# Performance work log

Measured on AMD Instinct MI355X. Metric: run time of the kernel, lower is better.

## Reference

```python
import jax, jax.numpy as jnp
import numpy as np

N_HEAD = 16
N_QUERY_GROUPS = 4
HEAD_SIZE = 128
ROPE_N_ELEM = 32
N_EMBD = 2048
LN_EPS = 1e-5


def _layernorm(x, w, b):
    mu = jnp.mean(x, axis=-1, keepdims=True)
    var = jnp.var(x, axis=-1, keepdims=True)
    return (x - mu) * jax.lax.rsqrt(var + LN_EPS) * w + b


def _apply_rope(x, cos, sin):
    # x: (B, H, T, ROPE_N_ELEM); cos/sin: (T, ROPE_N_ELEM) broadcast over B,H
    half = x.shape[-1] // 2
    x1, x2 = x[..., :half], x[..., half:]
    rotated = jnp.concatenate((-x2, x1), axis=-1)
    return x * cos + rotated * sin


def setup_inputs() -> dict:
    key = jax.random.key(0)
    ks = jax.random.split(key, 12)
    B, T, C = 2, 2048, N_EMBD
    qkv_out = (N_HEAD + 2 * N_QUERY_GROUPS) * HEAD_SIZE
    ffn = 4 * C
    s = lambda fan_in: 1.0 / np.sqrt(fan_in)
    # rope cache (lit-gpt build_rope_cache, base 10000)
    theta = 1.0 / (10000.0 ** (jnp.arange(0, ROPE_N_ELEM, 2, dtype=jnp.float32) / ROPE_N_ELEM))
    idx_theta = jnp.outer(jnp.arange(T, dtype=jnp.float32), theta)  # (T, ROPE/2)
    idx_theta = jnp.concatenate((idx_theta, idx_theta), axis=-1)    # (T, ROPE)
    return {
        'x': jax.random.normal(ks[0], (B, T, C), dtype=jnp.float32),
        'cos': jnp.cos(idx_theta),
        'sin': jnp.sin(idx_theta),
        'ln1_w': jnp.ones((C,), jnp.float32),
        'ln1_b': jnp.zeros((C,), jnp.float32),
        'w_qkv': jax.random.normal(ks[1], (C, qkv_out), jnp.float32) * s(C),
        'b_qkv': jnp.zeros((qkv_out,), jnp.float32),
        'w_proj': jax.random.normal(ks[2], (C, C), jnp.float32) * s(C),
        'b_proj': jnp.zeros((C,), jnp.float32),
        'ln2_w': jnp.ones((C,), jnp.float32),
        'ln2_b': jnp.zeros((C,), jnp.float32),
        'w_fc1': jax.random.normal(ks[3], (C, ffn), jnp.float32) * s(C),
        'b_fc1': jnp.zeros((ffn,), jnp.float32),
        'w_fc2': jax.random.normal(ks[4], (ffn, C), jnp.float32) * s(ffn),
        'b_fc2': jnp.zeros((C,), jnp.float32),
    }


def reference(x, cos, sin, ln1_w, ln1_b, w_qkv, b_qkv, w_proj, b_proj,
              ln2_w, ln2_b, w_fc1, b_fc1, w_fc2, b_fc2):
    B, T, C = x.shape
    q_per_kv = N_HEAD // N_QUERY_GROUPS
    D = HEAD_SIZE

    # LayerNormLinear: fused LN + QKV projection
    qkv = _layernorm(x, ln1_w, ln1_b) @ w_qkv + b_qkv           # (B,T,(H+2G)*D)
    qkv = qkv.reshape(B, T, N_QUERY_GROUPS, q_per_kv + 2, D)
    qkv = jnp.transpose(qkv, (0, 2, 3, 1, 4))                    # (B,G,q_per_kv+2,T,D)
    q = qkv[:, :, :q_per_kv]                                     # (B,G,q_per_kv,T,D)
    k = qkv[:, :, q_per_kv:q_per_kv + 1]                         # (B,G,1,T,D)
    v = qkv[:, :, q_per_kv + 1:]
    k = jnp.broadcast_to(k, (B, N_QUERY_GROUPS, q_per_kv, T, D))
    v = jnp.broadcast_to(v, (B, N_QUERY_GROUPS, q_per_kv, T, D))
    q = q.reshape(B, N_HEAD, T, D)
    k = k.reshape(B, N_HEAD, T, D)
    v = v.reshape(B, N_HEAD, T, D)

    # inline RoPE on first ROPE_N_ELEM channels
    q = jnp.concatenate((_apply_rope(q[..., :ROPE_N_ELEM], cos, sin), q[..., ROPE_N_ELEM:]), axis=-1)
    k = jnp.concatenate((_apply_rope(k[..., :ROPE_N_ELEM], cos, sin), k[..., ROPE_N_ELEM:]), axis=-1)

    # causal scaled dot-product attention
    scale = 1.0 / jnp.sqrt(jnp.asarray(D, q.dtype))
    scores = jnp.einsum('bhtd,bhsd->bhts', q, k) * scale          # (B,H,T,T)
    causal = jnp.tril(jnp.ones((T, T), dtype=bool))
    scores = jnp.where(causal, scores, jnp.finfo(scores.dtype).min)
    probs = jax.nn.softmax(scores, axis=-1)
    y = jnp.einsum('bhts,bhsd->bhtd', probs, v)                   # (B,H,T,D)
    y = jnp.transpose(y, (0, 2, 1, 3)).reshape(B, T, C)

    h = y @ w_proj + b_proj

    # parallel residual: x + attn + LayerNormMLP(x)
    mlp_in = _layernorm(x, ln2_w, ln2_b)
    mlp = jax.nn.gelu(mlp_in @ w_fc1 + b_fc1, approximate=False) @ w_fc2 + b_fc2
    return mlp + h + x
```

## Files before the change

### kernel.cpp

```cpp
#include <hip/hip_runtime.h>
#include <cstdint>
#include <cstddef>


typedef unsigned short u16;
typedef __bf16 bf16x8 __attribute__((ext_vector_type(8)));
typedef float  f32x4  __attribute__((ext_vector_type(4)));

#define B_      2
#define T_      2048
#define C_      2048
#define NH_     16
#define NG_     4
#define HD_     128
#define QKVO_   3072
#define FFN_    8192
#define ROWS_   4096

__device__ __forceinline__ u16 f2b(float f) {
  union { float f; uint32_t u; } c; c.f = f;
  uint32_t u = c.u;
  return (u16)((u + 0x7fffu + ((u >> 16) & 1u)) >> 16);
}
__device__ __forceinline__ float b2f(u16 h) {
  union { uint32_t u; float f; } c; c.u = ((uint32_t)h) << 16;
  return c.f;
}
__device__ __forceinline__ void load_lds16(const void* g, void* l) {
  __builtin_amdgcn_global_load_lds(
      (const __attribute__((address_space(1))) uint32_t*)g,
      (__attribute__((address_space(3))) uint32_t*)l, 16, 0, 0);
}

__global__ __launch_bounds__(256) void ln2x_kernel(
    const float* __restrict__ x,
    const float* __restrict__ w1, const float* __restrict__ b1,
    const float* __restrict__ w2, const float* __restrict__ b2,
    u16* __restrict__ o1, u16* __restrict__ o2)
{
  const int row = blockIdx.x;
  const float4* xr = (const float4*)(x + (size_t)row * C_);
  const int t = threadIdx.x;
  float4 v0 = xr[t];
  float4 v1 = xr[t + 256];
  float s  = v0.x + v0.y + v0.z + v0.w + v1.x + v1.y + v1.z + v1.w;
  float ss = v0.x*v0.x + v0.y*v0.y + v0.z*v0.z + v0.w*v0.w
           + v1.x*v1.x + v1.y*v1.y + v1.z*v1.z + v1.w*v1.w;
#pragma unroll
  for (int o = 32; o; o >>= 1) { s += __shfl_down(s, o); ss += __shfl_down(ss, o); }
  __shared__ float red[8];
  const int w = t >> 6;
  if ((t & 63) == 0) { red[w] = s; red[4 + w] = ss; }
  __syncthreads();
  s  = red[0] + red[1] + red[2] + red[3];
  ss = red[4] + red[5] + red[6] + red[7];
  const float mu   = s * (1.0f / C_);
  const float rstd = rsqrtf(ss * (1.0f / C_) - mu * mu + 1e-5f);

  const float4* W1 = (const float4*)w1; const float4* B1 = (const float4*)b1;
  const float4* W2 = (const float4*)w2; const float4* B2 = (const float4*)b2;
#pragma unroll
  for (int c = 0; c < 2; ++c) {
    const int idx = t + c * 256;
    float4 v = (c == 0) ? v0 : v1;
    float n0 = (v.x - mu) * rstd, n1 = (v.y - mu) * rstd;
    float n2 = (v.z - mu) * rstd, n3 = (v.w - mu) * rstd;
    float4 a1 = W1[idx], c1 = B1[idx], a2 = W2[idx], c2 = B2[idx];
    uint64_t p1 = (uint64_t)f2b(n0*a1.x + c1.x)
                | ((uint64_t)f2b(n1*a1.y + c1.y) << 16)
                | ((uint64_t)f2b(n2*a1.z + c1.z) << 32)
                | ((uint64_t)f2b(n3*a1.w + c1.w) << 48);
    uint64_t p2 = (uint64_t)f2b(n0*a2.x + c2.x)
                | ((uint64_t)f2b(n1*a2.y + c2.y) << 16)
                | ((uint64_t)f2b(n2*a2.z + c2.z) << 32)
                | ((uint64_t)f2b(n3*a2.w + c2.w) << 48);
    ((uint64_t*)o1)[(size_t)row * (C_/4) + idx] = p1;
    ((uint64_t*)o2)[(size_t)row * (C_/4) + idx] = p2;
  }
}

__global__ __launch_bounds__(256) void tcast64(
    const float* __restrict__ in, u16* __restrict__ out, int R, int Ccols)
{
  __shared__ u16 tileT[64 * 72];
  const int c0 = blockIdx.x * 64, r0 = blockIdx.y * 64;
  const int lin = threadIdx.x;
  {
    const int cI = (lin & 15) * 4, r = lin >> 4;
#pragma unroll
    for (int i = 0; i < 4; ++i) {
      const int rr = r + i * 16;
      float4 v = *(const float4*)(in + (size_t)(r0 + rr) * Ccols + c0 + cI);
      tileT[(cI + 0) * 72 + rr] = f2b(v.x);
      tileT[(cI + 1) * 72 + rr] = f2b(v.y);
      tileT[(cI + 2) * 72 + rr] = f2b(v.z);
      tileT[(cI + 3) * 72 + rr] = f2b(v.w);
    }
  }
  __syncthreads();
  {
    const int rr = (lin & 15) * 4, cc = lin >> 4;
#pragma unroll
    for (int i = 0; i < 4; ++i) {
      const int c = cc + i * 16;
      ushort4 pk = *(const ushort4*)(tileT + c * 72 + rr);
      *(ushort4*)(out + (size_t)(c0 + c) * R + r0 + rr) = pk;
    }
  }
}

__device__ __forceinline__ void gemm_loop(
    const u16* __restrict__ Ap, const u16* __restrict__ Bp,
    int K, int kbeg, int kend, f32x4 acc[4][4])
{
  __shared__ u16 As[128 * 32];
  __shared__ u16 Bs[128 * 32];
  const int tid = threadIdx.x;
  const int w = tid >> 6, lane = tid & 63, quad = lane >> 4, l16 = lane & 15;
  const int wm = w >> 1, wn = w & 1;
  const int rowS = tid >> 2, slotS = tid & 3;

  for (int k0 = kbeg; k0 < kend; k0 += 32) {
    __syncthreads();
#pragma unroll
    for (int i = 0; i < 2; ++i) {
      int row = rowS + i * 64;
      int chunk = slotS ^ ((row >> 1) & 3);
      load_lds16(Ap + (size_t)row * K + k0 + chunk * 8, (char*)As + i * 4096 + w * 1024);
      load_lds16(Bp + (size_t)row * K + k0 + chunk * 8, (char*)Bs + i * 4096 + w * 1024);
    }
    __syncthreads();

    bf16x8 af[4], bf[4];
#pragma unroll
    for (int mt = 0; mt < 4; ++mt) {
      int row = wm * 64 + mt * 16 + l16;
      int slot = quad ^ ((row >> 1) & 3);
      af[mt] = *(const bf16x8*)(As + row * 32 + slot * 8);
    }
#pragma unroll
    for (int nt = 0; nt < 4; ++nt) {
      int row = wn * 64 + nt * 16 + l16;
      int slot = quad ^ ((row >> 1) & 3);
      bf[nt] = *(const bf16x8*)(Bs + row * 32 + slot * 8);
    }
#pragma unroll
    for (int mt = 0; mt < 4; ++mt)
#pragma unroll
      for (int nt = 0; nt < 4; ++nt)
        acc[mt][nt] = __builtin_amdgcn_mfma_f32_16x16x32_bf16(af[mt], bf[nt], acc[mt][nt], 0, 0, 0);
  }
}

#define GEMM_PROLOGUE(KSTRIDE, KBEG, KEND)                                    \
  const int tid = threadIdx.x;                                                \
  const int w = tid >> 6, lane = tid & 63, quad = lane >> 4, l16 = lane & 15; \
  const int wm = w >> 1, wn = w & 1;                                          \
  const int m0 = blockIdx.y * 128, n0 = blockIdx.x * 128;                     \
  const f32x4 vzero = {0.f, 0.f, 0.f, 0.f};                                   \
  f32x4 acc[4][4];                                                            \
  _Pragma("unroll") for (int i = 0; i < 4; ++i)                               \
    _Pragma("unroll") for (int j = 0; j < 4; ++j) acc[i][j] = vzero;          \
  gemm_loop(A + (size_t)m0 * (KSTRIDE), Bt + (size_t)n0 * (KSTRIDE),          \
            (KSTRIDE), (KBEG), (KEND), acc);

__global__ __launch_bounds__(256, 2) void gemm_qkv(
    const u16* __restrict__ A, const u16* __restrict__ Bt,
    const float* __restrict__ bias,
    const float* __restrict__ cosb, const float* __restrict__ sinb,
    u16* __restrict__ qb, u16* __restrict__ kb, u16* __restrict__ vtb)
{
  GEMM_PROLOGUE(C_, 0, C_)
  const int slice = n0 >> 7;
  const int g = slice / 6, s = slice % 6;
  const int b = m0 >> 11;

#pragma unroll
  for (int mt = 0; mt < 4; ++mt) {
    const int rowbase = m0 + wm * 64 + mt * 16 + quad * 4;
    const int t0 = rowbase & 2047;
    float vv[4][4];
#pragma unroll
    for (int nt = 0; nt < 4; ++nt)
#pragma unroll
      for (int r = 0; r < 4; ++r)
        vv[nt][r] = acc[mt][nt][r] + bias[n0 + wn * 64 + nt * 16 + l16];

    if (s < 5 && wn == 0) {
#pragma unroll
      for (int r = 0; r < 4; ++r) {
        const int t = t0 + r;
        float cs0 = cosb[t * 32 + l16],      sn0 = sinb[t * 32 + l16];
        float cs1 = cosb[t * 32 + 16 + l16], sn1 = sinb[t * 32 + 16 + l16];
        float a = vv[0][r], c = vv[1][r];
        vv[0][r] = a * cs0 - c * sn0;
        vv[1][r] = c * cs1 + a * sn1;
      }
    }

    if (s < 4) {
      u16* dst = qb + (size_t)(b * NH_ + g * 4 + s) * T_ * HD_;
#pragma unroll
      for (int nt = 0; nt < 4; ++nt)
#pragma unroll
        for (int r = 0; r < 4; ++r)
          dst[(size_t)(t0 + r) * HD_ + wn * 64 + nt * 16 + l16] = f2b(vv[nt][r]);
    } else if (s == 4) {
      u16* dst = kb + (size_t)(b * NG_ + g) * T_ * HD_;
#pragma unroll
      for (int nt = 0; nt < 4; ++nt)
#pragma unroll
        for (int r = 0; r < 4; ++r)
          dst[(size_t)(t0 + r) * HD_ + wn * 64 + nt * 16 + l16] = f2b(vv[nt][r]);
    } else {
      u16* dst = vtb + (size_t)(b * NG_ + g) * HD_ * T_;
#pragma unroll
      for (int nt = 0; nt < 4; ++nt) {
        const int d = wn * 64 + nt * 16 + l16;
        ushort4 pk = { f2b(vv[nt][0]), f2b(vv[nt][1]), f2b(vv[nt][2]), f2b(vv[nt][3]) };
        *(ushort4*)(dst + (size_t)d * T_ + t0) = pk;
      }
    }
  }
}

__global__ __launch_bounds__(256, 2) void gemm_proj(
    const u16* __restrict__ A, const u16* __restrict__ Bt,
    const float* __restrict__ bias, const float* __restrict__ resid,
    float* __restrict__ outF)
{
  GEMM_PROLOGUE(C_, 0, C_)
#pragma unroll
  for (int mt = 0; mt < 4; ++mt)
#pragma unroll
    for (int nt = 0; nt < 4; ++nt)
#pragma unroll
      for (int r = 0; r < 4; ++r) {
        int row = m0 + wm * 64 + mt * 16 + quad * 4 + r;
        int col = n0 + wn * 64 + nt * 16 + l16;
        float v = acc[mt][nt][r] + bias[col] + resid[(size_t)row * C_ + col];
        outF[(size_t)row * C_ + col] = v;
      }
}

__global__ __launch_bounds__(256, 2) void gemm_fc1(
    const u16* __restrict__ A, const u16* __restrict__ Bt,
    const float* __restrict__ bias, u16* __restrict__ outB)
{
  GEMM_PROLOGUE(C_, 0, C_)
#pragma unroll
  for (int mt = 0; mt < 4; ++mt)
#pragma unroll
    for (int nt = 0; nt < 4; ++nt)
#pragma unroll
      for (int r = 0; r < 4; ++r) {
        int row = m0 + wm * 64 + mt * 16 + quad * 4 + r;
        int col = n0 + wn * 64 + nt * 16 + l16;
        float v = acc[mt][nt][r] + bias[col];
        v = 0.5f * v * (1.0f + erff(v * 0.70710678118654752f));
        outB[(size_t)row * FFN_ + col] = f2b(v);
      }
}

__global__ __launch_bounds__(256, 2) void gemm_fc2(
    const u16* __restrict__ A, const u16* __restrict__ Bt,
    const float* __restrict__ bias, float* __restrict__ outF,
    float* __restrict__ pbuf)
{
  const int kh = FFN_ / 2;
  const int kbeg = blockIdx.z * kh;
  GEMM_PROLOGUE(FFN_, kbeg, kbeg + kh)
#pragma unroll
  for (int mt = 0; mt < 4; ++mt)
#pragma unroll
    for (int nt = 0; nt < 4; ++nt)
#pragma unroll
      for (int r = 0; r < 4; ++r) {
        int row = m0 + wm * 64 + mt * 16 + quad * 4 + r;
        int col = n0 + wn * 64 + nt * 16 + l16;
        size_t idx = (size_t)row * C_ + col;
        if (blockIdx.z == 0)
          outF[idx] = acc[mt][nt][r] + bias[col] + outF[idx];
        else
          pbuf[idx] = acc[mt][nt][r];
      }
}

__global__ __launch_bounds__(256) void add_pbuf(
    float* __restrict__ out, const float* __restrict__ p)
{
  size_t i = ((size_t)blockIdx.x * 256 + threadIdx.x) * 4;
  float4 a = *(float4*)(out + i);
  float4 b = *(const float4*)(p + i);
  a.x += b.x; a.y += b.y; a.z += b.z; a.w += b.w;
  *(float4*)(out + i) = a;
}

__global__ __launch_bounds__(256, 2) void attn_kernel(
    const u16* __restrict__ qb, const u16* __restrict__ kb,
    const u16* __restrict__ vt, u16* __restrict__ y)
{
  __shared__ u16 Qs[64 * 128];
  __shared__ u16 Ks[64 * 128];
  __shared__ u16 Vs[128 * 64];
  __shared__ u16 Ps[4 * 16 * 64];

  const int tid = threadIdx.x;
  const int w = tid >> 6, lane = tid & 63, quad = lane >> 4, l16 = lane & 15;
  const int b = blockIdx.y >> 4, h = blockIdx.y & 15, g = h >> 2;
  const int q0 = blockIdx.x * 64;

  const u16* Qg = qb + (size_t)(b * NH_ + h) * T_ * HD_;
  const u16* Kg = kb + (size_t)(b * NG_ + g) * T_ * HD_;
  const u16* Vg = vt + (size_t)(b * NG_ + g) * HD_ * T_;

  {
    const int row = tid >> 4, slot = tid & 15;
#pragma unroll
    for (int i = 0; i < 4; ++i) {
      int r = row + i * 16;
      int chunk = slot ^ (r & 7);
      load_lds16(Qg + (size_t)(q0 + r) * HD_ + chunk * 8, (char*)Qs + i * 4096 + w * 1024);
    }
  }
  __syncthreads();

  bf16x8 aq[4];
#pragma unroll
  for (int kk = 0; kk < 4; ++kk) {
    int row = w * 16 + l16;
    int slot = (kk * 4 + quad) ^ (row & 7);
    aq[kk] = *(const bf16x8*)(Qs + row * 128 + slot * 8);
  }

  const f32x4 vzero = {0.f, 0.f, 0.f, 0.f};
  float m_run[4] = {-1e30f, -1e30f, -1e30f, -1e30f};
  float l_run[4] = {0.f, 0.f, 0.f, 0.f};
  f32x4 O[8];
#pragma unroll
  for (int nt = 0; nt < 8; ++nt) O[nt] = vzero;

  const float scale = 0.08838834764831845f;
  const int rowK = tid >> 4, slotK = tid & 15;
  const int rowV = tid >> 3, slotV = tid & 7;

  for (int j = 0; j <= (int)blockIdx.x; ++j) {
    const int kv0 = j * 64;
    __syncthreads();
#pragma unroll
    for (int i = 0; i < 4; ++i) {
      int r = rowK + i * 16;
      int chunk = slotK ^ (r & 7);
      load_lds16(Kg + (size_t)(kv0 + r) * HD_ + chunk * 8, (char*)Ks + i * 4096 + w * 1024);
    }
#pragma unroll
    for (int i = 0; i < 4; ++i) {
      int r = rowV + i * 32;
      int chunk = slotV ^ (r & 7);
      load_lds16(Vg + (size_t)r * T_ + kv0 + chunk * 8, (char*)Vs + i * 4096 + w * 1024);
    }
    __syncthreads();

    f32x4 S[4];
#pragma unroll
    for (int jn = 0; jn < 4; ++jn) {
      f32x4 a = vzero;
#pragma unroll
      for (int kk = 0; kk < 4; ++kk) {
        int row = jn * 16 + l16;
        int slot = (kk * 4 + quad) ^ (row & 7);
        bf16x8 bk = *(const bf16x8*)(Ks + row * 128 + slot * 8);
        a = __builtin_amdgcn_mfma_f32_16x16x32_bf16(aq[kk], bk, a, 0, 0, 0);
      }
      S[jn] = a;
    }

    if (j == (int)blockIdx.x) {
#pragma unroll
      for (int jn = 0; jn < 4; ++jn) {
        int col = kv0 + jn * 16 + l16;
#pragma unroll
        for (int r = 0; r < 4; ++r) {
          int qrow = q0 + w * 16 + quad * 4 + r;
          float v = S[jn][r] * scale;
          S[jn][r] = (col <= qrow) ? v : -1e30f;
        }
      }
    } else {
#pragma unroll
      for (int jn = 0; jn < 4; ++jn)
#pragma unroll
        for (int r = 0; r < 4; ++r) S[jn][r] *= scale;
    }

    float mx[4];
#pragma unroll
    for (int r = 0; r < 4; ++r)
      mx[r] = fmaxf(fmaxf(S[0][r], S[1][r]), fmaxf(S[2][r], S[3][r]));
#pragma unroll
    for (int d = 1; d < 16; d <<= 1)
#pragma unroll
      for (int r = 0; r < 4; ++r) mx[r] = fmaxf(mx[r], __shfl_xor(mx[r], d));

    float alpha[4];
#pragma unroll
    for (int r = 0; r < 4; ++r) {
      float mn = fmaxf(m_run[r], mx[r]);
      alpha[r] = __expf(m_run[r] - mn);
      m_run[r] = mn;
    }
    float rs[4] = {0.f, 0.f, 0.f, 0.f};
#pragma unroll
    for (int jn = 0; jn < 4; ++jn)
#pragma unroll
      for (int r = 0; r < 4; ++r) {
        float p = __expf(S[jn][r] - m_run[r]);
        S[jn][r] = p;
        rs[r] += p;
      }
#pragma unroll
    for (int d = 1; d < 16; d <<= 1)
#pragma unroll
      for (int r = 0; r < 4; ++r) rs[r] += __shfl_xor(rs[r], d);
#pragma unroll
    for (int r = 0; r < 4; ++r) l_run[r] = l_run[r] * alpha[r] + rs[r];
#pragma unroll
    for (int nt = 0; nt < 8; ++nt)
#pragma unroll
      for (int r = 0; r < 4; ++r) O[nt][r] *= alpha[r];

#pragma unroll
    for (int jn = 0; jn < 4; ++jn)
#pragma unroll
      for (int r = 0; r < 4; ++r) {
        int row = quad * 4 + r;
        int col = jn * 16 + l16;
        int slot = (col >> 3) ^ (row & 7);
        Ps[w * 1024 + row * 64 + slot * 8 + (col & 7)] = f2b(S[jn][r]);
      }

    bf16x8 ap[2];
#pragma unroll
    for (int kk = 0; kk < 2; ++kk) {
      int slot = (kk * 4 + quad) ^ (l16 & 7);
      ap[kk] = *(const bf16x8*)(Ps + w * 1024 + l16 * 64 + slot * 8);
    }
#pragma unroll
    for (int nt = 0; nt < 8; ++nt) {
#pragma unroll
      for (int kk = 0; kk < 2; ++kk) {
        int row = nt * 16 + l16;
        int slot = (kk * 4 + quad) ^ (row & 7);
        bf16x8 bv = *(const bf16x8*)(Vs + row * 64 + slot * 8);
        O[nt] = __builtin_amdgcn_mfma_f32_16x16x32_bf16(ap[kk], bv, O[nt], 0, 0, 0);
      }
    }
  }

#pragma unroll
  for (int r = 0; r < 4; ++r) {
    float inv = 1.0f / l_run[r];
    int t = q0 + w * 16 + quad * 4 + r;
    size_t base = (size_t)(b * T_ + t) * C_ + h * HD_;
#pragma unroll
    for (int nt = 0; nt < 8; ++nt)
      y[base + nt * 16 + l16] = f2b(O[nt][r] * inv);
  }
}

extern "C" void kernel_launch(void* const* d_in, const int* in_sizes, int n_in,
                              void* d_out, int out_size, void* d_ws, size_t ws_size,
                              hipStream_t stream)
{
  const float* x     = (const float*)d_in[0];
  const float* cosb  = (const float*)d_in[1];
  const float* sinb  = (const float*)d_in[2];
  const float* ln1w  = (const float*)d_in[3];
  const float* ln1b  = (const float*)d_in[4];
  const float* wqkv  = (const float*)d_in[5];
  const float* bqkv  = (const float*)d_in[6];
  const float* wproj = (const float*)d_in[7];
  const float* bproj = (const float*)d_in[8];
  const float* ln2w  = (const float*)d_in[9];
  const float* ln2b  = (const float*)d_in[10];
  const float* wfc1  = (const float*)d_in[11];
  const float* bfc1  = (const float*)d_in[12];
  const float* wfc2  = (const float*)d_in[13];
  const float* bfc2  = (const float*)d_in[14];
  float* out = (float*)d_out;

  char* ws = (char*)d_ws;
  const size_t MiB = 1ull << 20;
  u16*   ln1    = (u16*)  (ws + 0);
  u16*   ln2    = (u16*)  (ws + 16 * MiB);
  float* pbuf   = (float*)(ws + 0);
  size_t off = 32 * MiB;
  auto alloc = [&](size_t bytes) -> char* {
    char* p = ws + off;
    off += (bytes + 255) & ~(size_t)255;
    return p;
  };
  u16* wqkvT  = (u16*)alloc((size_t)QKVO_ * C_ * 2);
  u16* wprojT = (u16*)alloc((size_t)C_ * C_ * 2);
  u16* wfc1T  = (u16*)alloc((size_t)FFN_ * C_ * 2);
  u16* wfc2T  = (u16*)alloc((size_t)C_ * FFN_ * 2);
  u16* qbuf   = (u16*)alloc((size_t)B_ * NH_ * T_ * HD_ * 2);
  u16* kbuf   = (u16*)alloc((size_t)B_ * NG_ * T_ * HD_ * 2);
  u16* vtb    = (u16*)alloc((size_t)B_ * NG_ * HD_ * T_ * 2);
  u16* ybuf   = (u16*)alloc((size_t)ROWS_ * C_ * 2);
  u16* gbuf   = (u16*)alloc((size_t)ROWS_ * FFN_ * 2);
  if (off > ws_size) return;

  ln2x_kernel<<<dim3(ROWS_), dim3(256), 0, stream>>>(x, ln1w, ln1b, ln2w, ln2b, ln1, ln2);

  tcast64<<<dim3(QKVO_/64, C_/64),  dim3(256), 0, stream>>>(wqkv,  wqkvT,  C_,   QKVO_);
  tcast64<<<dim3(C_/64,   C_/64),   dim3(256), 0, stream>>>(wproj, wprojT, C_,   C_);
  tcast64<<<dim3(FFN_/64, C_/64),   dim3(256), 0, stream>>>(wfc1,  wfc1T,  C_,   FFN_);
  tcast64<<<dim3(C_/64,   FFN_/64), dim3(256), 0, stream>>>(wfc2,  wfc2T,  FFN_, C_);

  gemm_qkv<<<dim3(QKVO_/128, ROWS_/128), dim3(256), 0, stream>>>(
      ln1, wqkvT, bqkv, cosb, sinb, qbuf, kbuf, vtb);

  attn_kernel<<<dim3(T_/64, B_*NH_), dim3(256), 0, stream>>>(qbuf, kbuf, vtb, ybuf);

  gemm_proj<<<dim3(C_/128, ROWS_/128), dim3(256), 0, stream>>>(
      ybuf, wprojT, bproj, x, out);

  gemm_fc1<<<dim3(FFN_/128, ROWS_/128), dim3(256), 0, stream>>>(
      ln2, wfc1T, bfc1, gbuf);

  gemm_fc2<<<dim3(C_/128, ROWS_/128, 2), dim3(256), 0, stream>>>(
      gbuf, wfc2T, bfc2, out, pbuf);

  add_pbuf<<<dim3((ROWS_*C_)/1024), dim3(256), 0, stream>>>(out, pbuf);
}
```

Measured before the change: 900.7 us.

## Enlarge attention query tile with causal load pairing and XCD-aware GEMM block swizzle

The attention kernel now gives each block two 128-row query tiles, tile i and tile 15-i, so every block does the same amount of causal work. Each warp handles 32 query rows, which reuses each K/V tile load across twice as many rows, and the P scratch buffer now lives in the Q shared-memory region. Separately, the qkv, proj and fc2 GEMMs use a 1D grid remapped so that blocks scheduled on the same XCD cover a contiguous region of the output, aimed at better L2 reuse. In exchange the attention kernel uses more registers and launches far fewer blocks (256), which may hurt occupancy and the ability to fill the CUs.

```diff
diff --git a/kernel.cpp b/kernel.cpp
--- a/kernel.cpp
+++ b/kernel.cpp
@@ -152,11 +152,11 @@
   }
 }
 
-#define GEMM_PROLOGUE(KSTRIDE, KBEG, KEND)                                    \
+#define GEMM_PROLOGUE(KSTRIDE, KBEG, KEND, M0, N0)                            \
   const int tid = threadIdx.x;                                                \
   const int w = tid >> 6, lane = tid & 63, quad = lane >> 4, l16 = lane & 15; \
   const int wm = w >> 1, wn = w & 1;                                          \
-  const int m0 = blockIdx.y * 128, n0 = blockIdx.x * 128;                     \
+  const int m0 = (M0), n0 = (N0);                                             \
   const f32x4 vzero = {0.f, 0.f, 0.f, 0.f};                                   \
   f32x4 acc[4][4];                                                            \
   _Pragma("unroll") for (int i = 0; i < 4; ++i)                               \
@@ -164,13 +164,20 @@
   gemm_loop(A + (size_t)m0 * (KSTRIDE), Bt + (size_t)n0 * (KSTRIDE),          \
             (KSTRIDE), (KBEG), (KEND), acc);
 
+#define XCD_SWIZZLE(RM, RN)                                                   \
+  const int lin_ = blockIdx.x;                                                \
+  const int xcd_ = lin_ & 7, loc_ = lin_ >> 3;                                \
+  const int mb_ = (xcd_ >> 1) * (RM) + loc_ / (RN);                           \
+  const int nb_ = (xcd_ & 1) * (RN) + loc_ % (RN);
+
 __global__ __launch_bounds__(256, 2) void gemm_qkv(
     const u16* __restrict__ A, const u16* __restrict__ Bt,
     const float* __restrict__ bias,
     const float* __restrict__ cosb, const float* __restrict__ sinb,
     u16* __restrict__ qb, u16* __restrict__ kb, u16* __restrict__ vtb)
 {
-  GEMM_PROLOGUE(C_, 0, C_)
+  XCD_SWIZZLE(8, 12)
+  GEMM_PROLOGUE(C_, 0, C_, mb_ * 128, nb_ * 128)
   const int slice = n0 >> 7;
   const int g = slice / 6, s = slice % 6;
   const int b = m0 >> 11;
@@ -229,7 +236,8 @@
     const float* __restrict__ bias, const float* __restrict__ resid,
     float* __restrict__ outF)
 {
-  GEMM_PROLOGUE(C_, 0, C_)
+  XCD_SWIZZLE(8, 8)
+  GEMM_PROLOGUE(C_, 0, C_, mb_ * 128, nb_ * 128)
 #pragma unroll
   for (int mt = 0; mt < 4; ++mt)
 #pragma unroll
@@ -247,7 +255,7 @@
     const u16* __restrict__ A, const u16* __restrict__ Bt,
     const float* __restrict__ bias, u16* __restrict__ outB)
 {
-  GEMM_PROLOGUE(C_, 0, C_)
+  GEMM_PROLOGUE(C_, 0, C_, blockIdx.y * 128, blockIdx.x * 128)
 #pragma unroll
   for (int mt = 0; mt < 4; ++mt)
 #pragma unroll
@@ -267,9 +275,10 @@
     const float* __restrict__ bias, float* __restrict__ outF,
     float* __restrict__ pbuf)
 {
+  XCD_SWIZZLE(8, 8)
   const int kh = FFN_ / 2;
   const int kbeg = blockIdx.z * kh;
-  GEMM_PROLOGUE(FFN_, kbeg, kbeg + kh)
+  GEMM_PROLOGUE(FFN_, kbeg, kbeg + kh, mb_ * 128, nb_ * 128)
 #pragma unroll
   for (int mt = 0; mt < 4; ++mt)
 #pragma unroll
@@ -300,171 +309,195 @@
     const u16* __restrict__ qb, const u16* __restrict__ kb,
     const u16* __restrict__ vt, u16* __restrict__ y)
 {
-  __shared__ u16 Qs[64 * 128];
+  __shared__ u16 Qs[128 * 128];
   __shared__ u16 Ks[64 * 128];
   __shared__ u16 Vs[128 * 64];
-  __shared__ u16 Ps[4 * 16 * 64];
+  u16* Ps = Qs;
 
   const int tid = threadIdx.x;
   const int w = tid >> 6, lane = tid & 63, quad = lane >> 4, l16 = lane & 15;
   const int b = blockIdx.y >> 4, h = blockIdx.y & 15, g = h >> 2;
-  const int q0 = blockIdx.x * 64;
 
   const u16* Qg = qb + (size_t)(b * NH_ + h) * T_ * HD_;
   const u16* Kg = kb + (size_t)(b * NG_ + g) * T_ * HD_;
   const u16* Vg = vt + (size_t)(b * NG_ + g) * HD_ * T_;
 
-  {
-    const int row = tid >> 4, slot = tid & 15;
-#pragma unroll
-    for (int i = 0; i < 4; ++i) {
-      int r = row + i * 16;
-      int chunk = slot ^ (r & 7);
+  const f32x4 vzero = {0.f, 0.f, 0.f, 0.f};
+  const float scale = 0.08838834764831845f;
+  const int rowQ = tid >> 4, slotQ = tid & 15;
+  const int rowV = tid >> 3, slotV = tid & 7;
+
+#pragma unroll
+  for (int p = 0; p < 2; ++p) {
+    const int qt = p == 0 ? (int)blockIdx.x : 15 - (int)blockIdx.x;
+    const int q0 = qt * 128;
+
+    __syncthreads();
+#pragma unroll
+    for (int i = 0; i < 8; ++i) {
+      int r = rowQ + i * 16;
+      int chunk = slotQ ^ (r & 7);
       load_lds16(Qg + (size_t)(q0 + r) * HD_ + chunk * 8, (char*)Qs + i * 4096 + w * 1024);
     }
-  }
-  __syncthreads();
-
-  bf16x8 aq[4];
-#pragma unroll
-  for (int kk = 0; kk < 4; ++kk) {
-    int row = w * 16 + l16;
-    int slot = (kk * 4 + quad) ^ (row & 7);
-    aq[kk] = *(const bf16x8*)(Qs + row * 128 + slot * 8);
-  }
-
-  const f32x4 vzero = {0.f, 0.f, 0.f, 0.f};
-  float m_run[4] = {-1e30f, -1e30f, -1e30f, -1e30f};
-  float l_run[4] = {0.f, 0.f, 0.f, 0.f};
-  f32x4 O[8];
-#pragma unroll
-  for (int nt = 0; nt < 8; ++nt) O[nt] = vzero;
-
-  const float scale = 0.08838834764831845f;
-  const int rowK = tid >> 4, slotK = tid & 15;
-  const int rowV = tid >> 3, slotV = tid & 7;
-
-  for (int j = 0; j <= (int)blockIdx.x; ++j) {
-    const int kv0 = j * 64;
     __syncthreads();
-#pragma unroll
-    for (int i = 0; i < 4; ++i) {
-      int r = rowK + i * 16;
-      int chunk = slotK ^ (r & 7);
-      load_lds16(Kg + (size_t)(kv0 + r) * HD_ + chunk * 8, (char*)Ks + i * 4096 + w * 1024);
-    }
-#pragma unroll
-    for (int i = 0; i < 4; ++i) {
-      int r = rowV + i * 32;
-      int chunk = slotV ^ (r & 7);
-      load_lds16(Vg + (size_t)r * T_ + kv0 + chunk * 8, (char*)Vs + i * 4096 + w * 1024);
-    }
-    __syncthreads();
-
-    f32x4 S[4];
-#pragma unroll
-    for (int jn = 0; jn < 4; ++jn) {
-      f32x4 a = vzero;
+
+    bf16x8 aq[2][4];
+#pragma unroll
+    for (int rg = 0; rg < 2; ++rg)
 #pragma unroll
       for (int kk = 0; kk < 4; ++kk) {
-        int row = jn * 16 + l16;
+        int row = w * 32 + rg * 16 + l16;
         int slot = (kk * 4 + quad) ^ (row & 7);
-        bf16x8 bk = *(const bf16x8*)(Ks + row * 128 + slot * 8);
-        a = __builtin_amdgcn_mfma_f32_16x16x32_bf16(aq[kk], bk, a, 0, 0, 0);
-      }
-      S[jn] = a;
-    }
-
-    if (j == (int)blockIdx.x) {
+        aq[rg][kk] = *(const bf16x8*)(Qs + row * 128 + slot * 8);
+      }
+
+    float m_run[2][4], l_run[2][4];
+    f32x4 O[2][8];
+#pragma unroll
+    for (int rg = 0; rg < 2; ++rg)
+#pragma unroll
+      for (int r = 0; r < 4; ++r) { m_run[rg][r] = -1e30f; l_run[rg][r] = 0.f; }
+#pragma unroll
+    for (int rg = 0; rg < 2; ++rg)
+#pragma unroll
+      for (int nt = 0; nt < 8; ++nt) O[rg][nt] = vzero;
+
+    const int jmax = 2 * qt + 1;
+    for (int j = 0; j <= jmax; ++j) {
+      const int kv0 = j * 64;
+      __syncthreads();
+#pragma unroll
+      for (int i = 0; i < 4; ++i) {
+        int r = rowQ + i * 16;
+        int chunk = slotQ ^ (r & 7);
+        load_lds16(Kg + (size_t)(kv0 + r) * HD_ + chunk * 8, (char*)Ks + i * 4096 + w * 1024);
+      }
+#pragma unroll
+      for (int i = 0; i < 4; ++i) {
+        int r = rowV + i * 32;
+        int chunk = slotV ^ (r & 7);
+        load_lds16(Vg + (size_t)r * T_ + kv0 + chunk * 8, (char*)Vs + i * 4096 + w * 1024);
+      }
+      __syncthreads();
+
+      f32x4 S[2][4];
 #pragma unroll
       for (int jn = 0; jn < 4; ++jn) {
-        int col = kv0 + jn * 16 + l16;
+        f32x4 s0 = vzero, s1 = vzero;
+#pragma unroll
+        for (int kk = 0; kk < 4; ++kk) {
+          int row = jn * 16 + l16;
+          int slot = (kk * 4 + quad) ^ (row & 7);
+          bf16x8 bk = *(const bf16x8*)(Ks + row * 128 + slot * 8);
+          s0 = __builtin_amdgcn_mfma_f32_16x16x32_bf16(aq[0][kk], bk, s0, 0, 0, 0);
+          s1 = __builtin_amdgcn_mfma_f32_16x16x32_bf16(aq[1][kk], bk, s1, 0, 0, 0);
+        }
+        S[0][jn] = s0; S[1][jn] = s1;
+      }
+
+      if (j >= 2 * qt) {
+#pragma unroll
+        for (int rg = 0; rg < 2; ++rg)
+#pragma unroll
+          for (int jn = 0; jn < 4; ++jn) {
+            int col = kv0 + jn * 16 + l16;
+#pragma unroll
+            for (int r = 0; r < 4; ++r) {
+              int qrow = q0 + w * 32 + rg * 16 + quad * 4 + r;
+              float v = S[rg][jn][r] * scale;
+              S[rg][jn][r] = (col <= qrow) ? v : -1e30f;
+            }
+          }
+      } else {
+#pragma unroll
+        for (int rg = 0; rg < 2; ++rg)
+#pragma unroll
+          for (int jn = 0; jn < 4; ++jn)
+#pragma unroll
+            for (int r = 0; r < 4; ++r) S[rg][jn][r] *= scale;
+      }
+
+#pragma unroll
+      for (int rg = 0; rg < 2; ++rg) {
+        float mx[4];
+#pragma unroll
+        for (int r = 0; r < 4; ++r)
+          mx[r] = fmaxf(fmaxf(S[rg][0][r], S[rg][1][r]), fmaxf(S[rg][2][r], S[rg][3][r]));
+#pragma unroll
+        for (int d = 1; d < 16; d <<= 1)
+#pragma unroll
+          for (int r = 0; r < 4; ++r) mx[r] = fmaxf(mx[r], __shfl_xor(mx[r], d));
+
+        float alpha[4];
 #pragma unroll
         for (int r = 0; r < 4; ++r) {
-          int qrow = q0 + w * 16 + quad * 4 + r;
-          float v = S[jn][r] * scale;
-          S[jn][r] = (col <= qrow) ? v : -1e30f;
+          float mn = fmaxf(m_run[rg][r], mx[r]);
+          alpha[r] = __expf(m_run[rg][r] - mn);
+          m_run[rg][r] = mn;
         }
-      }
-    } else {
-#pragma unroll
-      for (int jn = 0; jn < 4; ++jn)
-#pragma unroll
-        for (int r = 0; r < 4; ++r) S[jn][r] *= scale;
-    }
-
-    float mx[4];
-#pragma unroll
-    for (int r = 0; r < 4; ++r)
-      mx[r] = fmaxf(fmaxf(S[0][r], S[1][r]), fmaxf(S[2][r], S[3][r]));
-#pragma unroll
-    for (int d = 1; d < 16; d <<= 1)
-#pragma unroll
-      for (int r = 0; r < 4; ++r) mx[r] = fmaxf(mx[r], __shfl_xor(mx[r], d));
-
-    float alpha[4];
-#pragma unroll
-    for (int r = 0; r < 4; ++r) {
-      float mn = fmaxf(m_run[r], mx[r]);
-      alpha[r] = __expf(m_run[r] - mn);
-      m_run[r] = mn;
-    }
-    float rs[4] = {0.f, 0.f, 0.f, 0.f};
-#pragma unroll
-    for (int jn = 0; jn < 4; ++jn)
+        float rs[4] = {0.f, 0.f, 0.f, 0.f};
+#pragma unroll
+        for (int jn = 0; jn < 4; ++jn)
+#pragma unroll
+          for (int r = 0; r < 4; ++r) {
+            float pv = __expf(S[rg][jn][r] - m_run[rg][r]);
+            S[rg][jn][r] = pv;
+            rs[r] += pv;
+          }
+#pragma unroll
+        for (int d = 1; d < 16; d <<= 1)
+#pragma unroll
+          for (int r = 0; r < 4; ++r) rs[r] += __shfl_xor(rs[r], d);
+#pragma unroll
+        for (int r = 0; r < 4; ++r) l_run[rg][r] = l_run[rg][r] * alpha[r] + rs[r];
+#pragma unroll
+        for (int nt = 0; nt < 8; ++nt)
+#pragma unroll
+          for (int r = 0; r < 4; ++r) O[rg][nt][r] *= alpha[r];
+
+#pragma unroll
+        for (int jn = 0; jn < 4; ++jn)
+#pragma unroll
+          for (int r = 0; r < 4; ++r) {
+            int row = quad * 4 + r;
+            int col = jn * 16 + l16;
+            int slot = (col >> 3) ^ (row & 7);
+            Ps[w * 2048 + rg * 1024 + row * 64 + slot * 8 + (col & 7)] = f2b(S[rg][jn][r]);
+          }
+      }
+
+      bf16x8 ap[2][2];
+#pragma unroll
+      for (int rg = 0; rg < 2; ++rg)
+#pragma unroll
+        for (int kk = 0; kk < 2; ++kk) {
+          int slot = (kk * 4 + quad) ^ (l16 & 7);
+          ap[rg][kk] = *(const bf16x8*)(Ps + w * 2048 + rg * 1024 + l16 * 64 + slot * 8);
+        }
+#pragma unroll
+      for (int nt = 0; nt < 8; ++nt) {
+#pragma unroll
+        for (int kk = 0; kk < 2; ++kk) {
+          int row = nt * 16 + l16;
+          int slot = (kk * 4 + quad) ^ (row & 7);
+          bf16x8 bv = *(const bf16x8*)(Vs + row * 64 + slot * 8);
+          O[0][nt] = __builtin_amdgcn_mfma_f32_16x16x32_bf16(ap[0][kk], bv, O[0][nt], 0, 0, 0);
+          O[1][nt] = __builtin_amdgcn_mfma_f32_16x16x32_bf16(ap[1][kk], bv, O[1][nt], 0, 0, 0);
+        }
+      }
+    }
+
+#pragma unroll
+    for (int rg = 0; rg < 2; ++rg)
 #pragma unroll
       for (int r = 0; r < 4; ++r) {
-        float p = __expf(S[jn][r] - m_run[r]);
-        S[jn][r] = p;
-        rs[r] += p;
-      }
-#pragma unroll
-    for (int d = 1; d < 16; d <<= 1)
-#pragma unroll
-      for (int r = 0; r < 4; ++r) rs[r] += __shfl_xor(rs[r], d);
-#pragma unroll
-    for (int r = 0; r < 4; ++r) l_run[r] = l_run[r] * alpha[r] + rs[r];
-#pragma unroll
-    for (int nt = 0; nt < 8; ++nt)
-#pragma unroll
-      for (int r = 0; r < 4; ++r) O[nt][r] *= alpha[r];
-
-#pragma unroll
-    for (int jn = 0; jn < 4; ++jn)
-#pragma unroll
-      for (int r = 0; r < 4; ++r) {
-        int row = quad * 4 + r;
-        int col = jn * 16 + l16;
-        int slot = (col >> 3) ^ (row & 7);
-        Ps[w * 1024 + row * 64 + slot * 8 + (col & 7)] = f2b(S[jn][r]);
-      }
-
-    bf16x8 ap[2];
-#pragma unroll
-    for (int kk = 0; kk < 2; ++kk) {
-      int slot = (kk * 4 + quad) ^ (l16 & 7);
-      ap[kk] = *(const bf16x8*)(Ps + w * 1024 + l16 * 64 + slot * 8);
-    }
-#pragma unroll
-    for (int nt = 0; nt < 8; ++nt) {
-#pragma unroll
-      for (int kk = 0; kk < 2; ++kk) {
-        int row = nt * 16 + l16;
-        int slot = (kk * 4 + quad) ^ (row & 7);
-        bf16x8 bv = *(const bf16x8*)(Vs + row * 64 + slot * 8);
-        O[nt] = __builtin_amdgcn_mfma_f32_16x16x32_bf16(ap[kk], bv, O[nt], 0, 0, 0);
-      }
-    }
-  }
-
-#pragma unroll
-  for (int r = 0; r < 4; ++r) {
-    float inv = 1.0f / l_run[r];
-    int t = q0 + w * 16 + quad * 4 + r;
-    size_t base = (size_t)(b * T_ + t) * C_ + h * HD_;
-#pragma unroll
-    for (int nt = 0; nt < 8; ++nt)
-      y[base + nt * 16 + l16] = f2b(O[nt][r] * inv);
+        float inv = 1.0f / l_run[rg][r];
+        int t = q0 + w * 32 + rg * 16 + quad * 4 + r;
+        size_t base = (size_t)(b * T_ + t) * C_ + h * HD_;
+#pragma unroll
+        for (int nt = 0; nt < 8; ++nt)
+          y[base + nt * 16 + l16] = f2b(O[rg][nt][r] * inv);
+      }
   }
 }
 
@@ -518,18 +551,18 @@
   tcast64<<<dim3(FFN_/64, C_/64),   dim3(256), 0, stream>>>(wfc1,  wfc1T,  C_,   FFN_);
   tcast64<<<dim3(C_/64,   FFN_/64), dim3(256), 0, stream>>>(wfc2,  wfc2T,  FFN_, C_);
 
-  gemm_qkv<<<dim3(QKVO_/128, ROWS_/128), dim3(256), 0, stream>>>(
+  gemm_qkv<<<dim3(768), dim3(256), 0, stream>>>(
       ln1, wqkvT, bqkv, cosb, sinb, qbuf, kbuf, vtb);
 
-  attn_kernel<<<dim3(T_/64, B_*NH_), dim3(256), 0, stream>>>(qbuf, kbuf, vtb, ybuf);
-
-  gemm_proj<<<dim3(C_/128, ROWS_/128), dim3(256), 0, stream>>>(
+  attn_kernel<<<dim3(8, B_*NH_), dim3(256), 0, stream>>>(qbuf, kbuf, vtb, ybuf);
+
+  gemm_proj<<<dim3(512), dim3(256), 0, stream>>>(
       ybuf, wprojT, bproj, x, out);
 
   gemm_fc1<<<dim3(FFN_/128, ROWS_/128), dim3(256), 0, stream>>>(
       ln2, wfc1T, bfc1, gbuf);
 
-  gemm_fc2<<<dim3(C_/128, ROWS_/128, 2), dim3(256), 0, stream>>>(
+  gemm_fc2<<<dim3(512, 1, 2), dim3(256), 0, stream>>>(
       gbuf, wfc2T, bfc2, out, pbuf);
 
   add_pbuf<<<dim3((ROWS_*C_)/1024), dim3(256), 0, stream>>>(out, pbuf);
```

After: 851.2 us. -5.5%, faster.
